# Kernel optimization log

Hardware: AMD Instinct MI355X
Metric: run time of the kernel (lower is better)

Reference implementation:

```python
import jax, jax.numpy as jnp
import numpy as np

D_MODEL = 1024
NUM_HEADS = 16
HEAD_DIM = D_MODEL // NUM_HEADS


def setup_inputs() -> dict:
    key = jax.random.key(0)
    ks = jax.random.split(key, 9)
    s = 1.0 / np.sqrt(D_MODEL)
    return {
        "x": jax.random.normal(ks[0], (4, 2048, D_MODEL), dtype=jnp.float32),
        "Wq": jax.random.uniform(ks[1], (D_MODEL, D_MODEL), minval=-s, maxval=s, dtype=jnp.float32),
        "bq": jax.random.uniform(ks[2], (D_MODEL,), minval=-s, maxval=s, dtype=jnp.float32),
        "Wk": jax.random.uniform(ks[3], (D_MODEL, D_MODEL), minval=-s, maxval=s, dtype=jnp.float32),
        "bk": jax.random.uniform(ks[4], (D_MODEL,), minval=-s, maxval=s, dtype=jnp.float32),
        "Wv": jax.random.uniform(ks[5], (D_MODEL, D_MODEL), minval=-s, maxval=s, dtype=jnp.float32),
        "bv": jax.random.uniform(ks[6], (D_MODEL,), minval=-s, maxval=s, dtype=jnp.float32),
        "Wo": jax.random.uniform(ks[7], (D_MODEL, D_MODEL), minval=-s, maxval=s, dtype=jnp.float32),
        "bo": jax.random.uniform(ks[8], (D_MODEL,), minval=-s, maxval=s, dtype=jnp.float32),
    }


def reference(x, Wq, bq, Wk, bk, Wv, bv, Wo, bo):
    B, T, C = x.shape
    H, Dh = NUM_HEADS, HEAD_DIM
    # projections (nn.Linear applies x @ W^T + b)
    q = (x @ Wq.T + bq).reshape(B, T, H, Dh).transpose(0, 2, 1, 3)  # [B,H,T,Dh]
    k = (x @ Wk.T + bk).reshape(B, T, H, Dh).transpose(0, 2, 1, 3)
    v = (x @ Wv.T + bv).reshape(B, T, H, Dh).transpose(0, 2, 1, 3)
    scale = 1.0 / np.sqrt(Dh).astype(np.float32)
    att = jnp.einsum("bhqd,bhkd->bhqk", q, k) * scale  # [B,H,T,T]
    causal = jnp.tril(jnp.ones((T, T), dtype=bool))
    att = jnp.where(causal[None, None], att, -jnp.inf)
    att = jax.nn.softmax(att, axis=-1)
    # dropout is identity in eval mode
    out = jnp.einsum("bhqk,bhkd->bhqd", att, v)  # [B,H,T,Dh]
    out = out.transpose(0, 2, 1, 3).reshape(B, T, C)
    return out @ Wo.T + bo
```

## Files before the change

kernel.cpp:

```cpp
#include <hip/hip_runtime.h>
#include <stdint.h>

typedef __attribute__((ext_vector_type(8))) short short8;
typedef __attribute__((ext_vector_type(4))) short short4v;
typedef __attribute__((ext_vector_type(4))) float floatx4;

#define QSCALE 0.1803368801111f

__device__ __forceinline__ unsigned short f2bf(float f) {
  unsigned int u = __float_as_uint(f);
  unsigned int r = (u + 0x7FFFu + ((u >> 16) & 1u)) >> 16;
  return (unsigned short)r;
}

__device__ __forceinline__ unsigned int cvt_pk_bf16(float lo, float hi) {
  unsigned int r;
  asm("v_cvt_pk_bf16_f32 %0, %1, %2" : "=v"(r) : "v"(lo), "v"(hi));
  return r;
}

__device__ __forceinline__ float max3f(float a, float b, float c) {
  float r;
  asm("v_max3_f32 %0, %1, %2, %3" : "=v"(r) : "v"(a), "v"(b), "v"(c));
  return r;
}

__device__ __forceinline__ float max16(const floatx4& a, const floatx4& b,
                                       const floatx4& c, const floatx4& d) {
  float m1 = max3f(a[0], a[1], a[2]);
  float m2 = max3f(a[3], b[0], b[1]);
  float m3 = max3f(b[2], b[3], c[0]);
  float m4 = max3f(c[1], c[2], c[3]);
  float m5 = max3f(d[0], d[1], d[2]);
  float r1 = max3f(m1, m2, m3);
  float r2 = max3f(m4, m5, d[3]);
  return fmaxf(r1, r2);
}

__device__ __forceinline__ void async_copy16(void* lds, const void* g) {
  __builtin_amdgcn_global_load_lds(
      (const __attribute__((address_space(1))) unsigned int*)g,
      (__attribute__((address_space(3))) unsigned int*)lds, 16, 0, 0);
}

__global__ __launch_bounds__(256) void f2ball_kernel(
    const float* __restrict__ x, unsigned short* __restrict__ xb,
    const float* __restrict__ w0, const float* __restrict__ w1,
    const float* __restrict__ w2, const float* __restrict__ w3,
    unsigned short* __restrict__ o0, unsigned short* __restrict__ o1,
    unsigned short* __restrict__ o2, unsigned short* __restrict__ o3) {
  const float* in;
  unsigned short* out;
  long i;
  if (blockIdx.x < 8192) {
    in = x;
    out = xb;
    i = (long)blockIdx.x * 256 + threadIdx.x;
  } else {
    int wb = blockIdx.x - 8192;
    int which = wb >> 10;
    in = (which == 0) ? w0 : (which == 1) ? w1 : (which == 2) ? w2 : w3;
    out = (which == 0) ? o0 : (which == 1) ? o1 : (which == 2) ? o2 : o3;
    i = (long)(wb & 1023) * 256 + threadIdx.x;
  }
  float4 v = ((const float4*)in)[i];
  short4v o;
  o[0] = (short)f2bf(v.x);
  o[1] = (short)f2bf(v.y);
  o[2] = (short)f2bf(v.z);
  o[3] = (short)f2bf(v.w);
  *(short4v*)(out + i * 4) = o;
}

__device__ __forceinline__ void gemm128_mainloop_db(
    const unsigned short* __restrict__ A, const unsigned short* __restrict__ Bt,
    int K, long brow, long bcol, unsigned short* As, unsigned short* Bs,
    floatx4 acc[4][4]) {
  const int tid = threadIdx.x;
  const int wave = tid >> 6;
  const int lane = tid & 63;
  const int wr = wave >> 1, wc = wave & 1;
  const int lr = lane & 15, lg = lane >> 4;

  const unsigned short* ga = A + (brow + (tid >> 2)) * (long)K + (tid & 3) * 8;
  const unsigned short* gb = Bt + (bcol + (tid >> 2)) * (long)K + (tid & 3) * 8;
  const int woff = wave * 512;
  const int a_off = (wr * 64 + lr) * 32 + lg * 8;
  const int b_off = (wc * 64 + lr) * 32 + lg * 8;

  async_copy16(As + woff, ga);
  async_copy16(As + woff + 2048, ga + (long)64 * K);
  async_copy16(Bs + woff, gb);
  async_copy16(Bs + woff + 2048, gb + (long)64 * K);
  ga += 32;
  gb += 32;
  __syncthreads();

  int buf = 0;
  for (int kt = 0; kt < K; kt += 32) {
    if (kt + 32 < K) {
      unsigned short* lA = As + (buf ^ 1) * 4096 + woff;
      unsigned short* lB = Bs + (buf ^ 1) * 4096 + woff;
      async_copy16(lA, ga);
      async_copy16(lA + 2048, ga + (long)64 * K);
      async_copy16(lB, gb);
      async_copy16(lB + 2048, gb + (long)64 * K);
      ga += 32;
      gb += 32;
    }
    const unsigned short* Ab = As + buf * 4096;
    const unsigned short* Bb = Bs + buf * 4096;
    short8 af[4], bf[4];
#pragma unroll
    for (int i = 0; i < 4; ++i) {
      af[i] = *(const short8*)(Ab + a_off + i * 512);
      bf[i] = *(const short8*)(Bb + b_off + i * 512);
    }
#pragma unroll
    for (int i = 0; i < 4; ++i)
#pragma unroll
      for (int j = 0; j < 4; ++j)
        acc[i][j] = __builtin_amdgcn_mfma_f32_16x16x32_bf16(af[i], bf[j], acc[i][j], 0, 0, 0);
    __syncthreads();
    buf ^= 1;
  }
}

__global__ __launch_bounds__(256, 2) void qkv_gemm256(
    const unsigned short* __restrict__ xb, const unsigned short* __restrict__ wqkv,
    const float* __restrict__ bq, const float* __restrict__ bk,
    const float* __restrict__ bv, unsigned short* __restrict__ q_out,
    unsigned short* __restrict__ k_out, unsigned short* __restrict__ vt_out) {
  __shared__ __align__(16) unsigned short Sh[24576];
  unsigned short* As = Sh;
  unsigned short* Bs = Sh + 8192;

  const int tid = threadIdx.x;
  const int wave = tid >> 6, lane = tid & 63;
  const int wr = wave >> 1, wc = wave & 1;
  const int lr = lane & 15, lg = lane >> 4;

  const long brow = (long)blockIdx.x * 128;
  const long bcol = (long)blockIdx.y * 256;

  floatx4 zero = {0.f, 0.f, 0.f, 0.f};
  floatx4 acc[4][8];
#pragma unroll
  for (int i = 0; i < 4; ++i)
#pragma unroll
    for (int j = 0; j < 8; ++j) acc[i][j] = zero;

  const int K = 1024;
  const unsigned short* ga = xb + (brow + (tid >> 2)) * (long)K + (tid & 3) * 8;
  const unsigned short* gb = wqkv + (bcol + (tid >> 2)) * (long)K + (tid & 3) * 8;
  const int woff = wave * 512;
  const int a_off = (wr * 64 + lr) * 32 + lg * 8;
  const int b_off = (wc * 128 + lr) * 32 + lg * 8;

  async_copy16(As + woff, ga);
  async_copy16(As + woff + 2048, ga + (long)64 * K);
#pragma unroll
  for (int jj = 0; jj < 4; ++jj)
    async_copy16(Bs + woff + jj * 2048, gb + (long)jj * 64 * K);
  ga += 32;
  gb += 32;
  __syncthreads();

  int buf = 0;
  for (int kt = 0; kt < K; kt += 32) {
    if (kt + 32 < K) {
      unsigned short* lA = As + (buf ^ 1) * 4096 + woff;
      unsigned short* lB = Bs + (buf ^ 1) * 8192 + woff;
      async_copy16(lA, ga);
      async_copy16(lA + 2048, ga + (long)64 * K);
#pragma unroll
      for (int jj = 0; jj < 4; ++jj)
        async_copy16(lB + jj * 2048, gb + (long)jj * 64 * K);
      ga += 32;
      gb += 32;
    }
    const unsigned short* Ab = As + buf * 4096;
    const unsigned short* Bb = Bs + buf * 8192;
    short8 av[4], bvf[8];
#pragma unroll
    for (int i = 0; i < 4; ++i) av[i] = *(const short8*)(Ab + a_off + i * 512);
#pragma unroll
    for (int j = 0; j < 8; ++j) bvf[j] = *(const short8*)(Bb + b_off + j * 512);
    __builtin_amdgcn_s_setprio(1);
#pragma unroll
    for (int i = 0; i < 4; ++i)
#pragma unroll
      for (int j = 0; j < 8; ++j)
        acc[i][j] = __builtin_amdgcn_mfma_f32_16x16x32_bf16(av[i], bvf[j], acc[i][j], 0, 0, 0);
    __builtin_amdgcn_s_setprio(0);
    __syncthreads();
    buf ^= 1;
  }

  const int kind = (int)(bcol >> 10);
  const float* bias = (kind == 0) ? bq : (kind == 1 ? bk : bv);

  if (kind == 2) {
#pragma unroll 1
    for (int half = 0; half < 2; ++half) {
      if (wc == half) {
#pragma unroll
        for (int i = 0; i < 4; ++i)
#pragma unroll
          for (int j = 0; j < 8; ++j) {
            int n_local = j * 16 + lr;
            int m_base = wr * 64 + i * 16 + lg * 4;
            float bsc = bias[(int)((bcol + half * 128 + n_local) & 1023)];
            short4v pk;
#pragma unroll
            for (int r = 0; r < 4; ++r) pk[r] = (short)f2bf(acc[i][j][r] + bsc);
            *(short4v*)(Sh + n_local * 136 + m_base) = pk;
          }
      }
      __syncthreads();
      const int b = (int)(brow >> 11);
      const int t0 = (int)(brow & 2047);
      const int f0h = (int)(bcol - 2048) + half * 128;
#pragma unroll
      for (int p = 0; p < 8; ++p) {
        int c = p * 256 + tid;
        int d_loc = c >> 4, tc = c & 15;
        short8 v = *(const short8*)(Sh + d_loc * 136 + tc * 8);
        int h = (f0h >> 6) + (d_loc >> 6);
        int d = d_loc & 63;
        *(short8*)(vt_out + ((long)((b * 16 + h) * 64 + d)) * 2048 + t0 + tc * 8) = v;
      }
      __syncthreads();
    }
  } else {
#pragma unroll
    for (int i = 0; i < 4; ++i)
#pragma unroll
      for (int j = 0; j < 8; ++j)
#pragma unroll
        for (int r = 0; r < 4; ++r) {
          int m = (int)brow + wr * 64 + i * 16 + lg * 4 + r;
          int n = (int)bcol + wc * 128 + j * 16 + lr;
          int f = n & 1023;
          float v = acc[i][j][r] + bias[f];
          if (kind == 0) v *= QSCALE;
          unsigned short o = f2bf(v);
          int h = f >> 6, d = f & 63;
          int bb = m >> 11, t = m & 2047;
          long bh = (long)(bb * 16 + h);
          if (kind == 0)
            q_out[(bh * 2048 + t) * 64 + d] = o;
          else
            k_out[(bh * 2048 + t) * 64 + d] = o;
        }
  }
}

__global__ __launch_bounds__(256, 4) void out_gemm(
    const unsigned short* __restrict__ ob, const unsigned short* __restrict__ wo,
    const float* __restrict__ bo, float* __restrict__ out) {
  __shared__ unsigned short As[2 * 128 * 32];
  __shared__ unsigned short Bs[2 * 128 * 32];
  floatx4 zero = {0.f, 0.f, 0.f, 0.f};
  floatx4 acc[4][4];
#pragma unroll
  for (int i = 0; i < 4; ++i)
#pragma unroll
    for (int j = 0; j < 4; ++j) acc[i][j] = zero;

  long brow = (long)blockIdx.x * 128;
  long bcol = (long)blockIdx.y * 128;
  gemm128_mainloop_db(ob, wo, 1024, brow, bcol, As, Bs, acc);

  const int wave = threadIdx.x >> 6, lane = threadIdx.x & 63;
  const int wr = wave >> 1, wc = wave & 1, lr = lane & 15, lg = lane >> 4;
#pragma unroll
  for (int i = 0; i < 4; ++i)
#pragma unroll
    for (int j = 0; j < 4; ++j)
#pragma unroll
      for (int r = 0; r < 4; ++r) {
        int m = (int)brow + wr * 64 + i * 16 + lg * 4 + r;
        int n = (int)bcol + wc * 64 + j * 16 + lr;
        out[(long)m * 1024 + n] = acc[i][j][r] + bo[n];
      }
}

__device__ __forceinline__ void stage_kv(char* __restrict__ Kb, char* __restrict__ Vb,
                                         const char* __restrict__ Kp,
                                         const char* __restrict__ Vt, int kv0,
                                         int tid) {
  const int wave = tid >> 6;
#pragma unroll
  for (int j = 0; j < 2; ++j) {
    int d = j * 256 + tid;
    int row = d >> 3, cc = d & 7;
    int gc = cc ^ (row & 7);
    const char* gk = Kp + (size_t)kv0 * 128 + row * 128 + gc * 16;
    async_copy16(Kb + (j * 256 + wave * 64) * 16, gk);
    const char* gv = Vt + (size_t)row * 4096 + (size_t)kv0 * 2 + gc * 16;
    async_copy16(Vb + (j * 256 + wave * 64) * 16, gv);
  }
}

__device__ __forceinline__ void attn_step(
    const char* __restrict__ Kb, const char* __restrict__ Vb,
    char* __restrict__ PTw, const short8 (&qf)[2][2],
    int kv0, int q0, int lr, int lg, bool diag,
    float (&m_i)[2], floatx4 (&accL)[2], floatx4 (&accO)[2][4]) {
  floatx4 zero = {0.f, 0.f, 0.f, 0.f};
  const int x7 = lr & 7;
  floatx4 s[2][4];
  __builtin_amdgcn_s_setprio(1);
#pragma unroll
  for (int nt = 0; nt < 4; ++nt) {
    const char* kr = Kb + (nt * 16 + lr) * 128;
    short8 kf0 = *(const short8*)(kr + ((lg ^ x7) * 16));
    short8 kf1 = *(const short8*)(kr + (((4 + lg) ^ x7) * 16));
#pragma unroll
    for (int qa = 0; qa < 2; ++qa) {
      floatx4 a = zero;
      a = __builtin_amdgcn_mfma_f32_16x16x32_bf16(kf0, qf[qa][0], a, 0, 0, 0);
      a = __builtin_amdgcn_mfma_f32_16x16x32_bf16(kf1, qf[qa][1], a, 0, 0, 0);
      s[qa][nt] = a;
    }
  }
  __builtin_amdgcn_s_setprio(0);

  if (diag) {
#pragma unroll
    for (int qa = 0; qa < 2; ++qa) {
      const int q = q0 + qa * 16 + lr;
#pragma unroll
      for (int nt = 0; nt < 4; ++nt)
#pragma unroll
        for (int r = 0; r < 4; ++r) {
          int kvi = kv0 + nt * 16 + lg * 4 + r;
          if (kvi > q) s[qa][nt][r] = -1e30f;
        }
    }
  }

  float pmax[2];
#pragma unroll
  for (int qa = 0; qa < 2; ++qa)
    pmax[qa] = max16(s[qa][0], s[qa][1], s[qa][2], s[qa][3]);

  float g = fmaxf(pmax[0] - m_i[0], pmax[1] - m_i[1]);
  if (__any(g > 11.5f)) {
#pragma unroll
    for (int qa = 0; qa < 2; ++qa) {
      float mx = fmaxf(pmax[qa], __shfl_xor(pmax[qa], 16));
      mx = fmaxf(mx, __shfl_xor(mx, 32));
      float mnew = fmaxf(m_i[qa], mx);
      float scl = exp2f(m_i[qa] - mnew);
      m_i[qa] = mnew;
#pragma unroll
      for (int r = 0; r < 4; ++r) {
        float so = __shfl(scl, lg * 4 + r);
        accL[qa][r] *= so;
#pragma unroll
        for (int dt = 0; dt < 4; ++dt) accO[qa][dt][r] *= so;
      }
    }
  }

#pragma unroll
  for (int qa = 0; qa < 2; ++qa) {
    char* prow = PTw + (qa * 16 + lr) * 128;
#pragma unroll
    for (int nt = 0; nt < 4; ++nt) {
      float p0 = exp2f(s[qa][nt][0] - m_i[qa]);
      float p1 = exp2f(s[qa][nt][1] - m_i[qa]);
      float p2 = exp2f(s[qa][nt][2] - m_i[qa]);
      float p3 = exp2f(s[qa][nt][3] - m_i[qa]);
      uint2 wv;
      wv.x = cvt_pk_bf16(p0, p1);
      wv.y = cvt_pk_bf16(p2, p3);
      *(uint2*)(prow + (((2 * nt + (lg >> 1)) ^ x7) * 16) + ((2 * lg) & 3) * 4) = wv;
    }
  }

  short8 ones;
#pragma unroll
  for (int j = 0; j < 8; ++j) ones[j] = (short)0x3F80;

  __builtin_amdgcn_s_setprio(1);
#pragma unroll
  for (int kk = 0; kk < 2; ++kk) {
    short8 pf0 = *(const short8*)(PTw + lr * 128 + (((4 * kk + lg) ^ x7) * 16));
    short8 pf1 = *(const short8*)(PTw + (16 + lr) * 128 + (((4 * kk + lg) ^ x7) * 16));
#pragma unroll
    for (int dt = 0; dt < 4; ++dt) {
      short8 vf = *(const short8*)(Vb + (dt * 16 + lr) * 128 + (((4 * kk + lg) ^ x7) * 16));
      accO[0][dt] = __builtin_amdgcn_mfma_f32_16x16x32_bf16(pf0, vf, accO[0][dt], 0, 0, 0);
      accO[1][dt] = __builtin_amdgcn_mfma_f32_16x16x32_bf16(pf1, vf, accO[1][dt], 0, 0, 0);
    }
    accL[0] = __builtin_amdgcn_mfma_f32_16x16x32_bf16(pf0, ones, accL[0], 0, 0, 0);
    accL[1] = __builtin_amdgcn_mfma_f32_16x16x32_bf16(pf1, ones, accL[1], 0, 0, 0);
  }
  __builtin_amdgcn_s_setprio(0);
}

__global__ __launch_bounds__(256, 3) void attn_fwd(
    const unsigned short* __restrict__ qb, const unsigned short* __restrict__ kb,
    const unsigned short* __restrict__ vtb, unsigned short* __restrict__ ob) {
  __shared__ __align__(16) char Kbuf[2][8192];
  __shared__ __align__(16) char Vbuf[2][8192];
  __shared__ __align__(16) char PTbuf[4][4096];

  const int id = blockIdx.x;
  const int qt = 15 - (id >> 6);
  const int bh = id & 63;

  const int tid = threadIdx.x;
  const int wave = tid >> 6, lane = tid & 63;
  const int lr = lane & 15, lg = lane >> 4;
  const unsigned short* Q = qb + (long)bh * 2048 * 64;
  const char* Kp = (const char*)(kb + (long)bh * 2048 * 64);
  const char* Vt = (const char*)(vtb + (long)bh * 64 * 2048);
  const int b = bh >> 4, h = bh & 15;
  char* PTw = PTbuf[wave];

  floatx4 zero = {0.f, 0.f, 0.f, 0.f};

  const int q0 = qt * 128 + wave * 32;
  const int nkv = 2 * qt + 2;

  short8 qf[2][2];
#pragma unroll
  for (int qa = 0; qa < 2; ++qa)
#pragma unroll
    for (int kk = 0; kk < 2; ++kk)
      qf[qa][kk] = *(const short8*)(Q + (q0 + qa * 16 + lr) * 64 + kk * 32 + lg * 8);

  floatx4 accO[2][4];
  floatx4 accL[2];
#pragma unroll
  for (int qa = 0; qa < 2; ++qa) {
    accL[qa] = zero;
#pragma unroll
    for (int dt = 0; dt < 4; ++dt) accO[qa][dt] = zero;
  }
  float m_i[2] = {-1e30f, -1e30f};

  stage_kv(Kbuf[0], Vbuf[0], Kp, Vt, 0, tid);
  __syncthreads();
#pragma unroll 1
  for (int kv = 0; kv < nkv; ++kv) {
    if (kv + 1 < nkv)
      stage_kv(Kbuf[(kv + 1) & 1], Vbuf[(kv + 1) & 1], Kp, Vt, (kv + 1) * 64, tid);
    const int kv0 = kv * 64;
    if (kv0 < q0 + 32)
      attn_step(Kbuf[kv & 1], Vbuf[kv & 1], PTw, qf, kv0, q0, lr, lg,
                kv0 + 64 > q0, m_i, accL, accO);
    __syncthreads();
  }

#pragma unroll
  for (int qa = 0; qa < 2; ++qa) {
#pragma unroll
    for (int r = 0; r < 4; ++r) {
      float io = 1.f / accL[qa][r];
      int tq = q0 + qa * 16 + 4 * lg + r;
#pragma unroll
      for (int dt = 0; dt < 4; ++dt)
        ob[((long)b * 2048 + tq) * 1024 + h * 64 + dt * 16 + lr] =
            f2bf(accO[qa][dt][r] * io);
    }
  }
}

extern "C" void kernel_launch(void* const* d_in, const int* in_sizes, int n_in,
                              void* d_out, int out_size, void* d_ws, size_t ws_size,
                              hipStream_t stream) {
  const float* x = (const float*)d_in[0];
  const float* bq = (const float*)d_in[2];
  const float* bk = (const float*)d_in[4];
  const float* bv = (const float*)d_in[6];
  const float* bo = (const float*)d_in[8];
  float* out = (float*)d_out;

  char* ws = (char*)d_ws;
  unsigned short* xb = (unsigned short*)(ws);
  unsigned short* wqkv = (unsigned short*)(ws + (16l << 20));
  unsigned short* wob = (unsigned short*)(ws + (22l << 20));
  unsigned short* qb = (unsigned short*)(ws + (24l << 20));
  unsigned short* kb = (unsigned short*)(ws + (40l << 20));
  unsigned short* vtb = (unsigned short*)(ws + (56l << 20));
  unsigned short* ob = (unsigned short*)(ws + (72l << 20));

  f2ball_kernel<<<12288, 256, 0, stream>>>(
      x, xb, (const float*)d_in[1], (const float*)d_in[3], (const float*)d_in[5],
      (const float*)d_in[7], wqkv, wqkv + (1l << 20), wqkv + (2l << 20), wob);

  qkv_gemm256<<<dim3(64, 12), 256, 0, stream>>>(xb, wqkv, bq, bk, bv, qb, kb, vtb);
  attn_fwd<<<1024, 256, 0, stream>>>(qb, kb, vtb, ob);
  out_gemm<<<dim3(64, 8), 256, 0, stream>>>(ob, wob, bo, out);
}
```

Baseline: 164.4 us.

## Switch attention to 32x32x16 MFMA with register-resident P via permlane swap

```diff
diff --git a/kernel.cpp b/kernel.cpp
--- a/kernel.cpp
+++ b/kernel.cpp
@@ -4,6 +4,7 @@
 typedef __attribute__((ext_vector_type(8))) short short8;
 typedef __attribute__((ext_vector_type(4))) short short4v;
 typedef __attribute__((ext_vector_type(4))) float floatx4;
+typedef __attribute__((ext_vector_type(16))) float floatx16;
 
 #define QSCALE 0.1803368801111f
 
@@ -23,18 +24,6 @@
   float r;
   asm("v_max3_f32 %0, %1, %2, %3" : "=v"(r) : "v"(a), "v"(b), "v"(c));
   return r;
-}
-
-__device__ __forceinline__ float max16(const floatx4& a, const floatx4& b,
-                                       const floatx4& c, const floatx4& d) {
-  float m1 = max3f(a[0], a[1], a[2]);
-  float m2 = max3f(a[3], b[0], b[1]);
-  float m3 = max3f(b[2], b[3], c[0]);
-  float m4 = max3f(c[1], c[2], c[3]);
-  float m5 = max3f(d[0], d[1], d[2]);
-  float r1 = max3f(m1, m2, m3);
-  float r2 = max3f(m4, m5, d[3]);
-  return fmaxf(r1, r2);
 }
 
 __device__ __forceinline__ void async_copy16(void* lds, const void* g) {
@@ -303,102 +292,97 @@
   }
 }
 
+__device__ __forceinline__ short8 read_frag(const char* __restrict__ base, int row,
+                                            int chunk) {
+  return *(const short8*)(base + row * 128 + ((chunk ^ (row & 7)) * 16));
+}
+
 __device__ __forceinline__ void attn_step(
     const char* __restrict__ Kb, const char* __restrict__ Vb,
-    char* __restrict__ PTw, const short8 (&qf)[2][2],
-    int kv0, int q0, int lr, int lg, bool diag,
-    float (&m_i)[2], floatx4 (&accL)[2], floatx4 (&accO)[2][4]) {
-  floatx4 zero = {0.f, 0.f, 0.f, 0.f};
-  const int x7 = lr & 7;
-  floatx4 s[2][4];
+    const short8 (&qf)[4], int kv0, int q0, int l31, int hi, bool diag,
+    float& m_i, float& l_i, floatx16 (&accO)[2]) {
+  floatx16 sh[2];
   __builtin_amdgcn_s_setprio(1);
 #pragma unroll
-  for (int nt = 0; nt < 4; ++nt) {
-    const char* kr = Kb + (nt * 16 + lr) * 128;
-    short8 kf0 = *(const short8*)(kr + ((lg ^ x7) * 16));
-    short8 kf1 = *(const short8*)(kr + (((4 + lg) ^ x7) * 16));
-#pragma unroll
-    for (int qa = 0; qa < 2; ++qa) {
-      floatx4 a = zero;
-      a = __builtin_amdgcn_mfma_f32_16x16x32_bf16(kf0, qf[qa][0], a, 0, 0, 0);
-      a = __builtin_amdgcn_mfma_f32_16x16x32_bf16(kf1, qf[qa][1], a, 0, 0, 0);
-      s[qa][nt] = a;
-    }
+  for (int hh = 0; hh < 2; ++hh) {
+    floatx16 a = {0.f};
+#pragma unroll
+    for (int e = 1; e < 16; ++e) a[e] = 0.f;
+#pragma unroll
+    for (int ks = 0; ks < 4; ++ks) {
+      short8 kf = read_frag(Kb, hh * 32 + l31, 2 * ks + hi);
+      a = __builtin_amdgcn_mfma_f32_32x32x16_bf16(kf, qf[ks], a, 0, 0, 0);
+    }
+    sh[hh] = a;
   }
   __builtin_amdgcn_s_setprio(0);
 
+  const int q = q0 + l31;
   if (diag) {
 #pragma unroll
-    for (int qa = 0; qa < 2; ++qa) {
-      const int q = q0 + qa * 16 + lr;
-#pragma unroll
-      for (int nt = 0; nt < 4; ++nt)
-#pragma unroll
-        for (int r = 0; r < 4; ++r) {
-          int kvi = kv0 + nt * 16 + lg * 4 + r;
-          if (kvi > q) s[qa][nt][r] = -1e30f;
-        }
-    }
-  }
-
-  float pmax[2];
-#pragma unroll
-  for (int qa = 0; qa < 2; ++qa)
-    pmax[qa] = max16(s[qa][0], s[qa][1], s[qa][2], s[qa][3]);
-
-  float g = fmaxf(pmax[0] - m_i[0], pmax[1] - m_i[1]);
-  if (__any(g > 11.5f)) {
-#pragma unroll
-    for (int qa = 0; qa < 2; ++qa) {
-      float mx = fmaxf(pmax[qa], __shfl_xor(pmax[qa], 16));
-      mx = fmaxf(mx, __shfl_xor(mx, 32));
-      float mnew = fmaxf(m_i[qa], mx);
-      float scl = exp2f(m_i[qa] - mnew);
-      m_i[qa] = mnew;
-#pragma unroll
-      for (int r = 0; r < 4; ++r) {
-        float so = __shfl(scl, lg * 4 + r);
-        accL[qa][r] *= so;
-#pragma unroll
-        for (int dt = 0; dt < 4; ++dt) accO[qa][dt][r] *= so;
+    for (int hh = 0; hh < 2; ++hh)
+#pragma unroll
+      for (int r = 0; r < 16; ++r) {
+        int kvi = kv0 + 32 * hh + (r & 3) + 8 * (r >> 2) + 4 * hi;
+        if (kvi > q) sh[hh][r] = -1e30f;
       }
-    }
-  }
-
-#pragma unroll
-  for (int qa = 0; qa < 2; ++qa) {
-    char* prow = PTw + (qa * 16 + lr) * 128;
-#pragma unroll
-    for (int nt = 0; nt < 4; ++nt) {
-      float p0 = exp2f(s[qa][nt][0] - m_i[qa]);
-      float p1 = exp2f(s[qa][nt][1] - m_i[qa]);
-      float p2 = exp2f(s[qa][nt][2] - m_i[qa]);
-      float p3 = exp2f(s[qa][nt][3] - m_i[qa]);
-      uint2 wv;
-      wv.x = cvt_pk_bf16(p0, p1);
-      wv.y = cvt_pk_bf16(p2, p3);
-      *(uint2*)(prow + (((2 * nt + (lg >> 1)) ^ x7) * 16) + ((2 * lg) & 3) * 4) = wv;
-    }
-  }
-
-  short8 ones;
-#pragma unroll
-  for (int j = 0; j < 8; ++j) ones[j] = (short)0x3F80;
+  }
+
+  float t[11];
+#pragma unroll
+  for (int i = 0; i < 10; ++i)
+    t[i] = max3f(sh[(3 * i) / 16][(3 * i) % 16], sh[(3 * i + 1) / 16][(3 * i + 1) % 16],
+                 sh[(3 * i + 2) / 16][(3 * i + 2) % 16]);
+  t[10] = fmaxf(sh[1][14], sh[1][15]);
+  float pmax = max3f(max3f(t[0], t[1], t[2]), max3f(t[3], t[4], t[5]),
+                     max3f(t[6], t[7], t[8]));
+  pmax = max3f(pmax, t[9], t[10]);
+
+  if (__any(pmax > m_i + 11.5f)) {
+    float mx = fmaxf(pmax, __shfl_xor(pmax, 32));
+    float mnew = fmaxf(m_i, mx);
+    float scl = exp2f(m_i - mnew);
+    m_i = mnew;
+    l_i *= scl;
+#pragma unroll
+    for (int dt = 0; dt < 2; ++dt)
+#pragma unroll
+      for (int r = 0; r < 16; ++r) accO[dt][r] *= scl;
+  }
+
+  float p[32];
+#pragma unroll
+  for (int hh = 0; hh < 2; ++hh)
+#pragma unroll
+    for (int r = 0; r < 16; ++r) p[hh * 16 + r] = exp2f(sh[hh][r] - m_i);
+  float ls = 0.f;
+#pragma unroll
+  for (int i = 0; i < 8; ++i)
+    ls += (p[4 * i] + p[4 * i + 1]) + (p[4 * i + 2] + p[4 * i + 3]);
+  l_i += ls;
+
+  short8 pb[4];
+#pragma unroll
+  for (int ks2 = 0; ks2 < 4; ++ks2) {
+    const int ib = (ks2 >> 1) * 16 + (ks2 & 1) * 8;
+    unsigned int a0 = cvt_pk_bf16(p[ib + 0], p[ib + 1]);
+    unsigned int b0 = cvt_pk_bf16(p[ib + 4], p[ib + 5]);
+    unsigned int a1 = cvt_pk_bf16(p[ib + 2], p[ib + 3]);
+    unsigned int b1 = cvt_pk_bf16(p[ib + 6], p[ib + 7]);
+    asm volatile("v_permlane32_swap_b32 %0, %1" : "+v"(a0), "+v"(b0));
+    asm volatile("v_permlane32_swap_b32 %0, %1" : "+v"(a1), "+v"(b1));
+    unsigned int w[4] = {a0, a1, b0, b1};
+    pb[ks2] = *(const short8*)w;
+  }
 
   __builtin_amdgcn_s_setprio(1);
 #pragma unroll
-  for (int kk = 0; kk < 2; ++kk) {
-    short8 pf0 = *(const short8*)(PTw + lr * 128 + (((4 * kk + lg) ^ x7) * 16));
-    short8 pf1 = *(const short8*)(PTw + (16 + lr) * 128 + (((4 * kk + lg) ^ x7) * 16));
-#pragma unroll
-    for (int dt = 0; dt < 4; ++dt) {
-      short8 vf = *(const short8*)(Vb + (dt * 16 + lr) * 128 + (((4 * kk + lg) ^ x7) * 16));
-      accO[0][dt] = __builtin_amdgcn_mfma_f32_16x16x32_bf16(pf0, vf, accO[0][dt], 0, 0, 0);
-      accO[1][dt] = __builtin_amdgcn_mfma_f32_16x16x32_bf16(pf1, vf, accO[1][dt], 0, 0, 0);
-    }
-    accL[0] = __builtin_amdgcn_mfma_f32_16x16x32_bf16(pf0, ones, accL[0], 0, 0, 0);
-    accL[1] = __builtin_amdgcn_mfma_f32_16x16x32_bf16(pf1, ones, accL[1], 0, 0, 0);
-  }
+  for (int dt = 0; dt < 2; ++dt)
+#pragma unroll
+    for (int ks2 = 0; ks2 < 4; ++ks2) {
+      short8 vf = read_frag(Vb, dt * 32 + l31, 2 * ks2 + hi);
+      accO[dt] = __builtin_amdgcn_mfma_f32_32x32x16_bf16(vf, pb[ks2], accO[dt], 0, 0, 0);
+    }
   __builtin_amdgcn_s_setprio(0);
 }
 
@@ -407,7 +391,6 @@
     const unsigned short* __restrict__ vtb, unsigned short* __restrict__ ob) {
   __shared__ __align__(16) char Kbuf[2][8192];
   __shared__ __align__(16) char Vbuf[2][8192];
-  __shared__ __align__(16) char PTbuf[4][4096];
 
   const int id = blockIdx.x;
   const int qt = 15 - (id >> 6);
@@ -415,34 +398,26 @@
 
   const int tid = threadIdx.x;
   const int wave = tid >> 6, lane = tid & 63;
-  const int lr = lane & 15, lg = lane >> 4;
+  const int l31 = lane & 31, hi = lane >> 5;
   const unsigned short* Q = qb + (long)bh * 2048 * 64;
   const char* Kp = (const char*)(kb + (long)bh * 2048 * 64);
   const char* Vt = (const char*)(vtb + (long)bh * 64 * 2048);
   const int b = bh >> 4, h = bh & 15;
-  char* PTw = PTbuf[wave];
-
-  floatx4 zero = {0.f, 0.f, 0.f, 0.f};
 
   const int q0 = qt * 128 + wave * 32;
   const int nkv = 2 * qt + 2;
 
-  short8 qf[2][2];
-#pragma unroll
-  for (int qa = 0; qa < 2; ++qa)
-#pragma unroll
-    for (int kk = 0; kk < 2; ++kk)
-      qf[qa][kk] = *(const short8*)(Q + (q0 + qa * 16 + lr) * 64 + kk * 32 + lg * 8);
-
-  floatx4 accO[2][4];
-  floatx4 accL[2];
-#pragma unroll
-  for (int qa = 0; qa < 2; ++qa) {
-    accL[qa] = zero;
-#pragma unroll
-    for (int dt = 0; dt < 4; ++dt) accO[qa][dt] = zero;
-  }
-  float m_i[2] = {-1e30f, -1e30f};
+  short8 qf[4];
+#pragma unroll
+  for (int ks = 0; ks < 4; ++ks)
+    qf[ks] = *(const short8*)(Q + (q0 + l31) * 64 + ks * 16 + hi * 8);
+
+  floatx16 accO[2];
+#pragma unroll
+  for (int dt = 0; dt < 2; ++dt)
+#pragma unroll
+    for (int r = 0; r < 16; ++r) accO[dt][r] = 0.f;
+  float m_i = -1e30f, l_i = 0.f;
 
   stage_kv(Kbuf[0], Vbuf[0], Kp, Vt, 0, tid);
   __syncthreads();
@@ -452,23 +427,24 @@
       stage_kv(Kbuf[(kv + 1) & 1], Vbuf[(kv + 1) & 1], Kp, Vt, (kv + 1) * 64, tid);
     const int kv0 = kv * 64;
     if (kv0 < q0 + 32)
-      attn_step(Kbuf[kv & 1], Vbuf[kv & 1], PTw, qf, kv0, q0, lr, lg,
-                kv0 + 64 > q0, m_i, accL, accO);
+      attn_step(Kbuf[kv & 1], Vbuf[kv & 1], qf, kv0, q0, l31, hi,
+                kv0 + 64 > q0, m_i, l_i, accO);
     __syncthreads();
   }
 
-#pragma unroll
-  for (int qa = 0; qa < 2; ++qa) {
-#pragma unroll
-    for (int r = 0; r < 4; ++r) {
-      float io = 1.f / accL[qa][r];
-      int tq = q0 + qa * 16 + 4 * lg + r;
-#pragma unroll
-      for (int dt = 0; dt < 4; ++dt)
-        ob[((long)b * 2048 + tq) * 1024 + h * 64 + dt * 16 + lr] =
-            f2bf(accO[qa][dt][r] * io);
-    }
-  }
+  float lt = l_i + __shfl_xor(l_i, 32);
+  float io = 1.f / lt;
+  const int q = q0 + l31;
+  unsigned short* orow = ob + ((long)b * 2048 + q) * 1024 + h * 64;
+#pragma unroll
+  for (int dt = 0; dt < 2; ++dt)
+#pragma unroll
+    for (int g = 0; g < 4; ++g) {
+      short4v pk;
+#pragma unroll
+      for (int e = 0; e < 4; ++e) pk[e] = (short)f2bf(accO[dt][4 * g + e] * io);
+      *(short4v*)(orow + dt * 32 + g * 8 + hi * 4) = pk;
+    }
 }
 
 extern "C" void kernel_launch(void* const* d_in, const int* in_sizes, int n_in,
```

After: 163.5 us. No clear change (-0.5%).
